# Performance work log

Hardware: AMD Instinct MI355X
Metric: run time of the kernel (lower is better)

Reference implementation:

```python
import jax, jax.numpy as jnp
import numpy as np

N = 50000
E = 800000
IN_DIM = 128
HIDDEN = 32
HEADS = 4
NUM_CLASSES = 10


def _glorot(key, shape):
    fan_in, fan_out = shape
    lim = float(np.sqrt(6.0 / (fan_in + fan_out)))
    return jax.random.uniform(key, shape, jnp.float32, -lim, lim)


def transformer_conv(x, src, dst, Wq, bq, Wk, bk, Wv, bv, Ws, bs, heads, out_ch, concat):
    """PyG TransformerConv (root_weight=True, beta=False, no edge_attr), eval mode."""
    n = x.shape[0]
    q = (x @ Wq + bq).reshape(n, heads, out_ch)
    k = (x @ Wk + bk).reshape(n, heads, out_ch)
    v = (x @ Wv + bv).reshape(n, heads, out_ch)
    # gather per-edge: query from target i, key/value from source j
    qe = q[dst]                                  # [E, H, C]
    ke = k[src]                                  # [E, H, C]
    ve = v[src]                                  # [E, H, C]
    logits = jnp.einsum('ehc,ehc->eh', qe, ke) / jnp.sqrt(jnp.float32(out_ch))
    # segment softmax over incoming edges of each target node
    m = jax.ops.segment_max(logits, dst, num_segments=n)        # [N, H]
    m = jnp.where(jnp.isfinite(m), m, 0.0)
    e = jnp.exp(logits - m[dst])                                # [E, H]
    denom = jax.ops.segment_sum(e, dst, num_segments=n)         # [N, H]
    alpha = e / (denom[dst] + 1e-16)                            # [E, H]
    agg = jax.ops.segment_sum(alpha[..., None] * ve, dst, num_segments=n)  # [N, H, C]
    if concat:
        out = agg.reshape(n, heads * out_ch)
    else:
        out = agg.mean(axis=1)
    return out + x @ Ws + bs  # root/skip connection


def setup_inputs() -> dict:
    key = jax.random.key(0)
    ks = jax.random.split(key, 20)
    x = jax.random.normal(ks[0], (N, IN_DIM), jnp.float32)
    edge_index = jax.random.randint(ks[1], (2, E), 0, N, jnp.int32)
    d1 = HEADS * HIDDEN  # conv1 per-head stacked width = 128
    params = {
        'Wq1': _glorot(ks[2], (IN_DIM, d1)), 'bq1': jnp.zeros((d1,), jnp.float32),
        'Wk1': _glorot(ks[3], (IN_DIM, d1)), 'bk1': jnp.zeros((d1,), jnp.float32),
        'Wv1': _glorot(ks[4], (IN_DIM, d1)), 'bv1': jnp.zeros((d1,), jnp.float32),
        'Ws1': _glorot(ks[5], (IN_DIM, d1)), 'bs1': jnp.zeros((d1,), jnp.float32),
        'Wq2': _glorot(ks[6], (d1, NUM_CLASSES)), 'bq2': jnp.zeros((NUM_CLASSES,), jnp.float32),
        'Wk2': _glorot(ks[7], (d1, NUM_CLASSES)), 'bk2': jnp.zeros((NUM_CLASSES,), jnp.float32),
        'Wv2': _glorot(ks[8], (d1, NUM_CLASSES)), 'bv2': jnp.zeros((NUM_CLASSES,), jnp.float32),
        'Ws2': _glorot(ks[9], (d1, NUM_CLASSES)), 'bs2': jnp.zeros((NUM_CLASSES,), jnp.float32),
    }
    return {'x': x, 'edge_index': edge_index, **params}


def reference(x, edge_index,
              Wq1, bq1, Wk1, bk1, Wv1, bv1, Ws1, bs1,
              Wq2, bq2, Wk2, bk2, Wv2, bv2, Ws2, bs2):
    src, dst = edge_index[0], edge_index[1]
    h = transformer_conv(x, src, dst, Wq1, bq1, Wk1, bk1, Wv1, bv1, Ws1, bs1,
                         HEADS, HIDDEN, concat=True)
    h = jax.nn.elu(h)
    # dropout is identity in eval mode
    out = transformer_conv(h, src, dst, Wq2, bq2, Wk2, bk2, Wv2, bv2, Ws2, bs2,
                           1, NUM_CLASSES, concat=False)
    return out
```

## Files before the change

### kernel.cpp

```cpp
#include <hip/hip_runtime.h>
#include <hip/hip_fp16.h>
#include <math.h>

#define NN 50000
#define EE 800000
#define NB 196

typedef _Float16 f16x8 __attribute__((ext_vector_type(8)));
typedef float f32x4 __attribute__((ext_vector_type(4)));
typedef float f32x2 __attribute__((ext_vector_type(2)));

__device__ inline float elu1(float x) { return x > 0.f ? x : expm1f(x); }

__global__ __launch_bounds__(256) void convert_x_deg(
    const float* __restrict__ x, __half* __restrict__ xh,
    const int* __restrict__ dst, int* __restrict__ deg)
{
    const int i = blockIdx.x * 256 + threadIdx.x;
    if (i < NN * 32) {
        const float4 v = ((const float4*)x)[i];
        ((__half2*)xh)[i * 2] = __floats2half2_rn(v.x, v.y);
        ((__half2*)xh)[i * 2 + 1] = __floats2half2_rn(v.z, v.w);
    }
    if (i < EE) atomicAdd(&deg[dst[i]], 1);
}

__global__ __launch_bounds__(256) void build_weights(
    const float* __restrict__ Wq, const float* __restrict__ Wk,
    const float* __restrict__ Wv, const float* __restrict__ Ws,
    const float* __restrict__ Wq2, const float* __restrict__ bq2,
    const float* __restrict__ Wk2, const float* __restrict__ bk2,
    const float* __restrict__ Wv2, const float* __restrict__ bv2,
    const float* __restrict__ Ws2, const float* __restrict__ bs2,
    __half* __restrict__ Wt, __half* __restrict__ W2t, float* __restrict__ bias2)
{
    const int idx = blockIdx.x * 256 + threadIdx.x;
    if (idx < 8192) {
        const int col = idx >> 7, k = idx & 127;
        const int m = col >> 4, j = col & 15;
        const float* W = m == 0 ? Wq2 : m == 1 ? Wk2 : m == 2 ? Wv2 : Ws2;
        W2t[idx] = (__half)(j < 10 ? W[k * 10 + j] : 0.f);
    }
    if (idx < 64) {
        const int m = idx >> 4, j = idx & 15;
        const float* b = m == 0 ? bq2 : m == 1 ? bk2 : m == 2 ? bv2 : bs2;
        bias2[idx] = j < 10 ? b[j] : 0.f;
    }
    __shared__ float tile[32][33];
    const int mat = blockIdx.x >> 4;
    const int tid = blockIdx.x & 15;
    const int k0 = (tid >> 2) * 32, c0 = (tid & 3) * 32;
    const float* W = mat == 0 ? Wq : mat == 1 ? Wk : mat == 2 ? Wv : Ws;
    const int r = threadIdx.x >> 5;
    const int c = threadIdx.x & 31;
    for (int rr = r; rr < 32; rr += 8) tile[rr][c] = W[(size_t)(k0 + rr) * 128 + c0 + c];
    __syncthreads();
    for (int rr = r; rr < 32; rr += 8)
        Wt[((size_t)mat * 128 + c0 + rr) * 128 + k0 + c] = (__half)tile[c][rr];
}

__global__ __launch_bounds__(256) void block_sums(
    const int* __restrict__ deg, int* __restrict__ bsum)
{
    __shared__ int ws[4];
    const int t = threadIdx.x;
    const int idx = blockIdx.x * 256 + t;
    int d = (idx < NN) ? deg[idx] : 0;
    #pragma unroll
    for (int off = 32; off; off >>= 1) d += __shfl_down(d, off, 64);
    if ((t & 63) == 0) ws[t >> 6] = d;
    __syncthreads();
    if (t == 0) bsum[blockIdx.x] = ws[0] + ws[1] + ws[2] + ws[3];
}

__global__ __launch_bounds__(256) void scan_bsums(int* __restrict__ bsum)
{
    __shared__ int s[256];
    const int t = threadIdx.x;
    int v = (t < NB) ? bsum[t] : 0;
    s[t] = v;
    __syncthreads();
    for (int off = 1; off < 256; off <<= 1) {
        int u = (t >= off) ? s[t - off] : 0;
        __syncthreads();
        s[t] += u;
        __syncthreads();
    }
    if (t < NB) bsum[t] = (t == 0) ? 0 : s[t - 1];
}

__global__ __launch_bounds__(256) void write_rowptr(
    const int* __restrict__ deg, const int* __restrict__ bsum,
    int* __restrict__ rowptr, int* __restrict__ cursor)
{
    __shared__ int s[256];
    const int t = threadIdx.x;
    const int idx = blockIdx.x * 256 + t;
    const int d = (idx < NN) ? deg[idx] : 0;
    s[t] = d;
    __syncthreads();
    for (int off = 1; off < 256; off <<= 1) {
        int u = (t >= off) ? s[t - off] : 0;
        __syncthreads();
        s[t] += u;
        __syncthreads();
    }
    const int excl = ((t == 0) ? 0 : s[t - 1]) + bsum[blockIdx.x];
    if (idx < NN) {
        rowptr[idx] = excl;
        cursor[idx] = excl;
    }
    if (idx == NN - 1) rowptr[NN] = excl + d;
}

__global__ __launch_bounds__(256) void scatter_edges(
    const int* __restrict__ src, const int* __restrict__ dst,
    int* __restrict__ cursor, int* __restrict__ esrc)
{
    const int e = blockIdx.x * 256 + threadIdx.x;
    if (e >= EE) return;
    const int d = dst[e];
    const int pos = atomicAdd(&cursor[d], 1);
    esrc[pos] = src[e];
}

__global__ __launch_bounds__(128) void gemm_l1_mfma(
    const __half* __restrict__ xh, const __half* __restrict__ Wt,
    const float* __restrict__ bq, const float* __restrict__ bk,
    const float* __restrict__ bv, const float* __restrict__ bs,
    __half* __restrict__ oqh, unsigned char* __restrict__ ok8,
    unsigned char* __restrict__ ov8, __half* __restrict__ osh)
{
    __shared__ __align__(16) unsigned char ldsraw[128 * 272];
    const int pair = blockIdx.y;
    const int t = threadIdx.x;
    const int wave = t >> 6;
    const int lane = t & 63;
    const int l = lane & 15;
    const int g = lane >> 4;
    const int brow0 = blockIdx.x * 128;
    const int wrow0 = brow0 + wave * 64;

    f16x8 xf[4][4];
    #pragma unroll
    for (int rt = 0; rt < 4; ++rt) {
        int arow = wrow0 + rt * 16 + l;
        if (arow >= NN) arow = NN - 1;
        #pragma unroll
        for (int kk = 0; kk < 4; ++kk)
            xf[rt][kk] = *(const f16x8*)((const _Float16*)xh + (size_t)arow * 128 + kk * 32 + g * 8);
    }

    for (int mi = 0; mi < 2; ++mi) {
        const int mat = pair * 2 + mi;
        const bool isfp8 = (mat == 1 || mat == 2);
        const float* b = mat == 0 ? bq : mat == 1 ? bk : mat == 2 ? bv : bs;
        const _Float16* wt = (const _Float16*)Wt + (size_t)mat * 128 * 128;

        f16x8 wf[4], wfn[4];
        #pragma unroll
        for (int kk = 0; kk < 4; ++kk)
            wf[kk] = *(const f16x8*)(wt + (size_t)l * 128 + kk * 32 + g * 8);

        for (int ct = 0; ct < 8; ++ct) {
            if (ct < 7) {
                const int ncol = (ct + 1) * 16 + l;
                #pragma unroll
                for (int kk = 0; kk < 4; ++kk)
                    wfn[kk] = *(const f16x8*)(wt + (size_t)ncol * 128 + kk * 32 + g * 8);
            }
            f32x4 acc[4];
            #pragma unroll
            for (int rt = 0; rt < 4; ++rt) acc[rt] = (f32x4){0.f, 0.f, 0.f, 0.f};
            #pragma unroll
            for (int kk = 0; kk < 4; ++kk)
                #pragma unroll
                for (int rt = 0; rt < 4; ++rt)
                    acc[rt] = __builtin_amdgcn_mfma_f32_16x16x32_f16(wf[kk], xf[rt][kk], acc[rt], 0, 0, 0);

            const int col0 = ct * 16 + g * 4;
            const float4 bias = *(const float4*)(b + col0);
            #pragma unroll
            for (int rt = 0; rt < 4; ++rt) {
                const int lrow = wave * 64 + rt * 16 + l;
                const float r0 = acc[rt][0] + bias.x;
                const float r1 = acc[rt][1] + bias.y;
                const float r2 = acc[rt][2] + bias.z;
                const float r3 = acc[rt][3] + bias.w;
                if (isfp8) {
                    int p = __builtin_amdgcn_cvt_pk_fp8_f32(r0, r1, 0, false);
                    p = __builtin_amdgcn_cvt_pk_fp8_f32(r2, r3, p, true);
                    *(int*)&ldsraw[lrow * 144 + col0] = p;
                } else {
                    __half2 h01 = __floats2half2_rn(r0, r1);
                    __half2 h23 = __floats2half2_rn(r2, r3);
                    uint2 u;
                    u.x = *(unsigned*)&h01;
                    u.y = *(unsigned*)&h23;
                    *(uint2*)&ldsraw[lrow * 272 + col0 * 2] = u;
                }
            }
            #pragma unroll
            for (int kk = 0; kk < 4; ++kk) wf[kk] = wfn[kk];
        }

        __syncthreads();
        if (isfp8) {
            unsigned char* o = (mat == 1) ? ok8 : ov8;
            #pragma unroll
            for (int i = 0; i < 8; ++i) {
                const int idx = i * 128 + t;
                const int row = idx >> 3;
                const int seg = idx & 7;
                const int grow = brow0 + row;
                if (grow < NN)
                    *(uint4*)(o + (size_t)grow * 128 + seg * 16) = *(const uint4*)&ldsraw[row * 144 + seg * 16];
            }
        } else {
            __half* o = (mat == 0) ? oqh : osh;
            #pragma unroll
            for (int i = 0; i < 16; ++i) {
                const int idx = i * 128 + t;
                const int row = idx >> 4;
                const int seg = idx & 15;
                const int grow = brow0 + row;
                if (grow < NN)
                    *(uint4*)(o + (size_t)grow * 128 + seg * 8) = *(const uint4*)&ldsraw[row * 272 + seg * 16];
            }
        }
        __syncthreads();
    }
}

__global__ __launch_bounds__(256) void node_attn1(
    const __half* __restrict__ q1, const unsigned char* __restrict__ k8,
    const unsigned char* __restrict__ v8,
    const int* __restrict__ rowptr, const int* __restrict__ esrc,
    const __half* __restrict__ skiph,
    __half* __restrict__ hb)
{
    const int t = threadIdx.x;
    const int wid = __builtin_amdgcn_readfirstlane(t >> 6);
    const int d = blockIdx.x * 4 + wid;
    if (d >= NN) return;
    const int lane = t & 63;
    const int ch2 = lane << 1;

    const int beg = rowptr[d];
    const int end = rowptr[d + 1];

    float2 qv = __half22float2(*(const __half2*)(q1 + (size_t)d * 128 + ch2));
    qv.x *= 0.17677669529663687f;
    qv.y *= 0.17677669529663687f;

    float2 accA = make_float2(0.f, 0.f), accB = make_float2(0.f, 0.f);
    float sA = 0.f, sB = 0.f;

    int i = beg;
    int sa = (i < end) ? esrc[i] : 0;
    int sb = (i + 1 < end) ? esrc[i + 1] : 0;
    unsigned kA = *(const unsigned short*)(k8 + (size_t)sa * 128 + ch2);
    unsigned vA = *(const unsigned short*)(v8 + (size_t)sa * 128 + ch2);
    unsigned kB = *(const unsigned short*)(k8 + (size_t)sb * 128 + ch2);
    unsigned vB = *(const unsigned short*)(v8 + (size_t)sb * 128 + ch2);

    while (i + 1 < end) {
        const int ni = i + 2;
        const int nsa = (ni < end) ? esrc[ni] : 0;
        const int nsb = (ni + 1 < end) ? esrc[ni + 1] : 0;
        const unsigned nkA = *(const unsigned short*)(k8 + (size_t)nsa * 128 + ch2);
        const unsigned nvA = *(const unsigned short*)(v8 + (size_t)nsa * 128 + ch2);
        const unsigned nkB = *(const unsigned short*)(k8 + (size_t)nsb * 128 + ch2);
        const unsigned nvB = *(const unsigned short*)(v8 + (size_t)nsb * 128 + ch2);

        const f32x2 kAf = __builtin_amdgcn_cvt_pk_f32_fp8((int)kA, false);
        const f32x2 kBf = __builtin_amdgcn_cvt_pk_f32_fp8((int)kB, false);
        const f32x2 vAf = __builtin_amdgcn_cvt_pk_f32_fp8((int)vA, false);
        const f32x2 vBf = __builtin_amdgcn_cvt_pk_f32_fp8((int)vB, false);

        float pA = qv.x * kAf[0] + qv.y * kAf[1];
        float pB = qv.x * kBf[0] + qv.y * kBf[1];
        pA += __shfl_xor(pA, 8, 16); pB += __shfl_xor(pB, 8, 16);
        pA += __shfl_xor(pA, 4, 16); pB += __shfl_xor(pB, 4, 16);
        pA += __shfl_xor(pA, 2, 16); pB += __shfl_xor(pB, 2, 16);
        pA += __shfl_xor(pA, 1, 16); pB += __shfl_xor(pB, 1, 16);

        const float exA = __expf(pA - 4.0f);
        accA.x += exA * vAf[0];
        accA.y += exA * vAf[1];
        sA += exA;

        const float exB = __expf(pB - 4.0f);
        accB.x += exB * vBf[0];
        accB.y += exB * vBf[1];
        sB += exB;

        kA = nkA; vA = nvA; kB = nkB; vB = nvB;
        i = ni;
    }
    if (i < end) {
        const f32x2 kAf = __builtin_amdgcn_cvt_pk_f32_fp8((int)kA, false);
        const f32x2 vAf = __builtin_amdgcn_cvt_pk_f32_fp8((int)vA, false);
        float pA = qv.x * kAf[0] + qv.y * kAf[1];
        pA += __shfl_xor(pA, 8, 16);
        pA += __shfl_xor(pA, 4, 16);
        pA += __shfl_xor(pA, 2, 16);
        pA += __shfl_xor(pA, 1, 16);
        const float exA = __expf(pA - 4.0f);
        accA.x += exA * vAf[0];
        accA.y += exA * vAf[1];
        sA += exA;
    }

    const float inv = 1.f / (sA + sB + 1e-16f);
    float2 o = __half22float2(*(const __half2*)(skiph + (size_t)d * 128 + ch2));
    o.x = elu1(o.x + (accA.x + accB.x) * inv);
    o.y = elu1(o.y + (accA.y + accB.y) * inv);
    *(__half2*)(hb + (size_t)d * 128 + ch2) = __floats2half2_rn(o.x, o.y);
}

__global__ __launch_bounds__(128) void node_l2_mfma(
    const __half* __restrict__ hb, const __half* __restrict__ W2t,
    const float* __restrict__ bias2,
    __half* __restrict__ q2h, __half* __restrict__ kv2h,
    float* __restrict__ out)
{
    const int t = threadIdx.x;
    const int wave = t >> 6;
    const int lane = t & 63;
    const int l = lane & 15;
    const int g = lane >> 4;
    const int wrow0 = blockIdx.x * 128 + wave * 64;
    if (wrow0 >= NN) return;
    const bool full = (wrow0 + 64 <= NN);

    f16x8 hf[4][4];
    #pragma unroll
    for (int rt = 0; rt < 4; ++rt) {
        int arow = wrow0 + rt * 16 + l;
        if (!full && arow >= NN) arow = NN - 1;
        #pragma unroll
        for (int kk = 0; kk < 4; ++kk)
            hf[rt][kk] = *(const f16x8*)((const _Float16*)hb + (size_t)arow * 128 + kk * 32 + g * 8);
    }

    #pragma unroll
    for (int ct = 0; ct < 4; ++ct) {
        const int col = ct * 16 + l;
        f16x8 wf[4];
        #pragma unroll
        for (int kk = 0; kk < 4; ++kk)
            wf[kk] = *(const f16x8*)((const _Float16*)W2t + (size_t)col * 128 + kk * 32 + g * 8);

        f32x4 acc[4];
        #pragma unroll
        for (int rt = 0; rt < 4; ++rt) acc[rt] = (f32x4){0.f, 0.f, 0.f, 0.f};
        #pragma unroll
        for (int kk = 0; kk < 4; ++kk)
            #pragma unroll
            for (int rt = 0; rt < 4; ++rt)
                acc[rt] = __builtin_amdgcn_mfma_f32_16x16x32_f16(wf[kk], hf[rt][kk], acc[rt], 0, 0, 0);

        const int c0 = g * 4;
        const float4 bias = *(const float4*)(bias2 + ct * 16 + c0);
        #pragma unroll
        for (int rt = 0; rt < 4; ++rt) {
            const int row = wrow0 + rt * 16 + l;
            if (full || row < NN) {
                float4 r;
                r.x = acc[rt][0] + bias.x;
                r.y = acc[rt][1] + bias.y;
                r.z = acc[rt][2] + bias.z;
                r.w = acc[rt][3] + bias.w;
                if (ct == 3) {
                    if (g < 2) {
                        *(float4*)(out + (size_t)row * 10 + c0) = r;
                    } else if (g == 2) {
                        out[(size_t)row * 10 + 8] = r.x;
                        out[(size_t)row * 10 + 9] = r.y;
                    }
                } else {
                    __half* p = ct == 0 ? q2h + (size_t)row * 16 + c0
                              : kv2h + (size_t)row * 32 + (ct == 2 ? 16 : 0) + c0;
                    __half2 h01 = __floats2half2_rn(r.x, r.y);
                    __half2 h23 = __floats2half2_rn(r.z, r.w);
                    uint2 u;
                    u.x = *(unsigned*)&h01;
                    u.y = *(unsigned*)&h23;
                    *(uint2*)p = u;
                }
            }
        }
    }
}

__global__ __launch_bounds__(256) void node_attn2(
    const __half* __restrict__ q2h, const __half* __restrict__ kv2h,
    const int* __restrict__ rowptr, const int* __restrict__ esrc,
    float* __restrict__ out)
{
    const int t = threadIdx.x;
    const int d = blockIdx.x * 32 + (t >> 3);
    if (d >= NN) return;
    const int c = t & 7;
    const int beg = rowptr[d];
    const int end = rowptr[d + 1];

    float2 qv = __half22float2(*(const __half2*)(q2h + (size_t)d * 16 + 2 * c));
    qv.x *= 0.31622776601683794f;
    qv.y *= 0.31622776601683794f;

    float2 acc[4];
    float ss[4];
    #pragma unroll
    for (int j = 0; j < 4; ++j) { acc[j] = make_float2(0.f, 0.f); ss[j] = 0.f; }

    int i = beg;
    __half2 kr[4], vr[4];
    #pragma unroll
    for (int j = 0; j < 4; ++j) {
        const int s = (i + j < end) ? esrc[i + j] : 0;
        kr[j] = *(const __half2*)(kv2h + (size_t)s * 32 + 2 * c);
        vr[j] = *(const __half2*)(kv2h + (size_t)s * 32 + 16 + 2 * c);
    }

    while (i + 3 < end) {
        const int ni = i + 4;
        __half2 nk[4], nv[4];
        #pragma unroll
        for (int j = 0; j < 4; ++j) {
            const int s = (ni + j < end) ? esrc[ni + j] : 0;
            nk[j] = *(const __half2*)(kv2h + (size_t)s * 32 + 2 * c);
            nv[j] = *(const __half2*)(kv2h + (size_t)s * 32 + 16 + 2 * c);
        }
        #pragma unroll
        for (int j = 0; j < 4; ++j) {
            const float2 kf = __half22float2(kr[j]);
            const float2 vf = __half22float2(vr[j]);
            float p = qv.x * kf.x + qv.y * kf.y;
            p += __shfl_xor(p, 4, 8);
            p += __shfl_xor(p, 2, 8);
            p += __shfl_xor(p, 1, 8);
            const float ex = __expf(p - 2.0f);
            acc[j].x += ex * vf.x;
            acc[j].y += ex * vf.y;
            ss[j] += ex;
        }
        #pragma unroll
        for (int j = 0; j < 4; ++j) { kr[j] = nk[j]; vr[j] = nv[j]; }
        i = ni;
    }
    for (; i < end; ++i) {
        const int s = esrc[i];
        const float2 kf = __half22float2(*(const __half2*)(kv2h + (size_t)s * 32 + 2 * c));
        const float2 vf = __half22float2(*(const __half2*)(kv2h + (size_t)s * 32 + 16 + 2 * c));
        float p = qv.x * kf.x + qv.y * kf.y;
        p += __shfl_xor(p, 4, 8);
        p += __shfl_xor(p, 2, 8);
        p += __shfl_xor(p, 1, 8);
        const float ex = __expf(p - 2.0f);
        acc[0].x += ex * vf.x;
        acc[0].y += ex * vf.y;
        ss[0] += ex;
    }

    if (c < 5) {
        const float ssum = ss[0] + ss[1] + ss[2] + ss[3];
        const float inv = 1.f / (ssum + 1e-16f);
        float2 o = *(float2*)(out + (size_t)d * 10 + 2 * c);
        o.x += (acc[0].x + acc[1].x + acc[2].x + acc[3].x) * inv;
        o.y += (acc[0].y + acc[1].y + acc[2].y + acc[3].y) * inv;
        *(float2*)(out + (size_t)d * 10 + 2 * c) = o;
    }
}

extern "C" void kernel_launch(void* const* d_in, const int* in_sizes, int n_in,
                              void* d_out, int out_size, void* d_ws, size_t ws_size,
                              hipStream_t stream) {
    const float* x   = (const float*)d_in[0];
    const int*   ei  = (const int*)d_in[1];
    const float* Wq1 = (const float*)d_in[2];  const float* bq1 = (const float*)d_in[3];
    const float* Wk1 = (const float*)d_in[4];  const float* bk1 = (const float*)d_in[5];
    const float* Wv1 = (const float*)d_in[6];  const float* bv1 = (const float*)d_in[7];
    const float* Ws1 = (const float*)d_in[8];  const float* bs1 = (const float*)d_in[9];
    const float* Wq2 = (const float*)d_in[10]; const float* bq2 = (const float*)d_in[11];
    const float* Wk2 = (const float*)d_in[12]; const float* bk2 = (const float*)d_in[13];
    const float* Wv2 = (const float*)d_in[14]; const float* bv2 = (const float*)d_in[15];
    const float* Ws2 = (const float*)d_in[16]; const float* bs2 = (const float*)d_in[17];
    float* out = (float*)d_out;

    const int* src = ei;
    const int* dst = ei + EE;

    __half* xh    = (__half*)d_ws;
    __half* q1h   = xh + (size_t)NN * 128;
    __half* skiph = q1h + (size_t)NN * 128;
    __half* hb    = skiph + (size_t)NN * 128;
    unsigned char* k8 = (unsigned char*)(hb + (size_t)NN * 128);
    unsigned char* v8 = k8 + (size_t)NN * 128;
    __half* Wt    = (__half*)(v8 + (size_t)NN * 128);
    __half* W2t   = Wt + 4 * 128 * 128;
    __half* q2h   = W2t + 64 * 128;
    __half* kv2h  = q2h + (size_t)NN * 16;
    float* bias2  = (float*)(kv2h + (size_t)NN * 32);
    int* deg      = (int*)(bias2 + 64);
    int* rowptr   = deg + NN;
    int* cursor   = rowptr + NN + 1;
    int* bsum     = cursor + NN;
    int* esrc     = bsum + NB;

    hipMemsetAsync(deg, 0, (size_t)NN * sizeof(int), stream);
    convert_x_deg<<<(NN * 32 + 255) / 256, 256, 0, stream>>>(x, xh, dst, deg);
    build_weights<<<64, 256, 0, stream>>>(Wq1, Wk1, Wv1, Ws1,
                                          Wq2, bq2, Wk2, bk2, Wv2, bv2, Ws2, bs2,
                                          Wt, W2t, bias2);

    block_sums<<<NB, 256, 0, stream>>>(deg, bsum);
    scan_bsums<<<1, 256, 0, stream>>>(bsum);
    write_rowptr<<<NB, 256, 0, stream>>>(deg, bsum, rowptr, cursor);
    scatter_edges<<<EE / 256, 256, 0, stream>>>(src, dst, cursor, esrc);

    gemm_l1_mfma<<<dim3((NN + 127) / 128, 2), 128, 0, stream>>>(
        xh, Wt, bq1, bk1, bv1, bs1, q1h, k8, v8, skiph);

    node_attn1<<<NN / 4, 256, 0, stream>>>(q1h, k8, v8, rowptr, esrc, skiph, hb);

    node_l2_mfma<<<(NN + 127) / 128, 128, 0, stream>>>(hb, W2t, bias2, q2h, kv2h, out);

    node_attn2<<<(NN + 31) / 32, 256, 0, stream>>>(q2h, kv2h, rowptr, esrc, out);
}
```

Baseline: 207.0 us.

## Replace per-edge global atomic CSR scatter with two-pass bucketed counting sort

Edges are no longer scattered into CSR order with one global atomic per edge on a per-node cursor. A first kernel bins edge chunks into 128 destination buckets in LDS, packing src and dst into one 16-bit pair per edge. A second kernel, one block per bucket, scatters into esrc using LDS atomics on local cursors. This aims to cut global atomic traffic and random writes, but it adds an extra kernel launch, an intermediate buffer, and only 128 blocks in the second pass. The packing relies on node ids fitting in 16 bits, which holds for N=50000.

After: 191.2 us. -7.7%, faster.

```diff
diff --git a/kernel.cpp b/kernel.cpp
--- a/kernel.cpp
+++ b/kernel.cpp
@@ -5,6 +5,9 @@
 #define NN 50000
 #define EE 800000
 #define NB 196
+#define NBK 128
+#define BKN 391
+#define CH 4096
 
 typedef _Float16 f16x8 __attribute__((ext_vector_type(8)));
 typedef float f32x4 __attribute__((ext_vector_type(4)));
@@ -91,7 +94,7 @@
 
 __global__ __launch_bounds__(256) void write_rowptr(
     const int* __restrict__ deg, const int* __restrict__ bsum,
-    int* __restrict__ rowptr, int* __restrict__ cursor)
+    int* __restrict__ rowptr, int* __restrict__ bcur)
 {
     __shared__ int s[256];
     const int t = threadIdx.x;
@@ -108,20 +111,73 @@
     const int excl = ((t == 0) ? 0 : s[t - 1]) + bsum[blockIdx.x];
     if (idx < NN) {
         rowptr[idx] = excl;
-        cursor[idx] = excl;
+        if (idx % BKN == 0) bcur[idx / BKN] = excl;
     }
     if (idx == NN - 1) rowptr[NN] = excl + d;
 }
 
-__global__ __launch_bounds__(256) void scatter_edges(
+__global__ __launch_bounds__(256) void bucket_stage(
     const int* __restrict__ src, const int* __restrict__ dst,
-    int* __restrict__ cursor, int* __restrict__ esrc)
-{
-    const int e = blockIdx.x * 256 + threadIdx.x;
-    if (e >= EE) return;
-    const int d = dst[e];
-    const int pos = atomicAdd(&cursor[d], 1);
-    esrc[pos] = src[e];
+    int* __restrict__ bcur, unsigned* __restrict__ bpair)
+{
+    __shared__ unsigned ep[CH];
+    __shared__ unsigned short eb[CH];
+    __shared__ unsigned stg[CH];
+    __shared__ int cnt[NBK], off[NBK], pos[NBK], gbase[NBK];
+    const int t = threadIdx.x;
+    const int e0 = blockIdx.x * CH;
+    const int n = min(CH, EE - e0);
+    if (t < NBK) cnt[t] = 0;
+    __syncthreads();
+    for (int i = t; i < n; i += 256) {
+        const int s = src[e0 + i], d = dst[e0 + i];
+        ep[i] = (unsigned)s | ((unsigned)d << 16);
+        const int b = d / BKN;
+        eb[i] = (unsigned short)b;
+        atomicAdd(&cnt[b], 1);
+    }
+    __syncthreads();
+    if (t == 0) {
+        int run = 0;
+        for (int b = 0; b < NBK; ++b) { off[b] = run; pos[b] = run; run += cnt[b]; }
+    }
+    __syncthreads();
+    if (t < NBK && cnt[t] > 0) gbase[t] = atomicAdd(&bcur[t], cnt[t]);
+    __syncthreads();
+    for (int i = t; i < n; i += 256) {
+        const int b = eb[i];
+        const int p = atomicAdd(&pos[b], 1);
+        stg[p] = ep[i];
+    }
+    __syncthreads();
+    for (int i = t; i < n; i += 256) {
+        int lo = 0, hi = NBK - 1;
+        while (lo < hi) { const int mid = (lo + hi + 1) >> 1; if (off[mid] <= i) lo = mid; else hi = mid - 1; }
+        bpair[gbase[lo] + (i - off[lo])] = stg[i];
+    }
+}
+
+__global__ __launch_bounds__(256) void bucket_scatter(
+    const unsigned* __restrict__ bpair, const int* __restrict__ rowptr,
+    int* __restrict__ esrc)
+{
+    __shared__ int lcur[BKN];
+    const int b = blockIdx.x;
+    const int n0 = b * BKN;
+    const int n1 = min(NN, n0 + BKN);
+    const int nn = n1 - n0;
+    const int t = threadIdx.x;
+    for (int i = t; i < nn; i += 256) lcur[i] = rowptr[n0 + i];
+    __syncthreads();
+    const int ebeg = rowptr[n0];
+    const int eend = rowptr[n1];
+    for (int i = ebeg + t; i < eend; i += 256) {
+        const unsigned p = bpair[i];
+        const int s = (int)(p & 0xFFFFu);
+        const int d = (int)(p >> 16);
+        const int pos = atomicAdd(&lcur[d - n0], 1);
+        esrc[pos] = s;
+    }
 }
 
 __global__ __launch_bounds__(128) void gemm_l1_mfma(
@@ -505,9 +561,10 @@
     float* bias2  = (float*)(kv2h + (size_t)NN * 32);
     int* deg      = (int*)(bias2 + 64);
     int* rowptr   = deg + NN;
-    int* cursor   = rowptr + NN + 1;
-    int* bsum     = cursor + NN;
+    int* bcur     = rowptr + NN + 1;
+    int* bsum     = bcur + NBK;
     int* esrc     = bsum + NB;
+    unsigned* bpair = (unsigned*)(esrc + EE);
 
     hipMemsetAsync(deg, 0, (size_t)NN * sizeof(int), stream);
     convert_x_deg<<<(NN * 32 + 255) / 256, 256, 0, stream>>>(x, xh, dst, deg);
@@ -517,8 +574,9 @@
 
     block_sums<<<NB, 256, 0, stream>>>(deg, bsum);
     scan_bsums<<<1, 256, 0, stream>>>(bsum);
-    write_rowptr<<<NB, 256, 0, stream>>>(deg, bsum, rowptr, cursor);
-    scatter_edges<<<EE / 256, 256, 0, stream>>>(src, dst, cursor, esrc);
+    write_rowptr<<<NB, 256, 0, stream>>>(deg, bsum, rowptr, bcur);
+    bucket_stage<<<(EE + CH - 1) / CH, 256, 0, stream>>>(src, dst, bcur, bpair);
+    bucket_scatter<<<NBK, 256, 0, stream>>>(bpair, rowptr, esrc);
 
     gemm_l1_mfma<<<dim3((NN + 127) / 128, 2), 128, 0, stream>>>(
         xh, Wt, bq1, bk1, bv1, bs1, q1h, k8, v8, skiph);
```
